# Kernel tuning notes

Measured on AMD Instinct MI355X. Metric: run time of the kernel, lower is better.

Reference implementation:

```python
import jax, jax.numpy as jnp
import numpy as np

B, S, D, O, R, E = 2, 4096, 4096, 4096, 256, 8
SCALE = 2.0

def setup_inputs() -> dict:
    key = jax.random.key(0)
    k_x, k_t, k_w, k_a, k_b = jax.random.split(key, 5)
    x = jax.random.normal(k_x, (B, S, D), dtype=jnp.float32)
    token_type = jax.random.randint(k_t, (S,), 0, E, dtype=jnp.int64)
    # weight_base: [out_features, in_features] as required by F.linear
    weight_base = jax.random.normal(k_w, (O, D), dtype=jnp.float32) * 0.02
    # LoRA stacks: lora_A [E, D, R], lora_B [E, R, O]. (Original inits B to zeros;
    # we use small random values so the LoRA path is numerically non-trivial.)
    lora_A = jax.random.normal(k_a, (E, D, R), dtype=jnp.float32) * 0.02
    lora_B = jax.random.normal(k_b, (E, R, O), dtype=jnp.float32) * 0.02
    return {"x": x, "weight_base": weight_base, "lora_A": lora_A,
            "lora_B": lora_B, "token_type": token_type}

def reference(x, weight_base, lora_A, lora_B, token_type):
    # base GEMM: F.linear(x, W) = x @ W.T  -> [B, S, O]
    base = jnp.einsum('bsd,od->bso', x, weight_base)
    # per-expert low-rank projection: h[e,b,s,:] = x[b,s,:] @ lora_A[e]
    h = jnp.einsum('bsd,edr->ebsr', x, lora_A)              # [E, B, S, R]
    # dispatch: zero out tokens not routed to expert e (token_type partitions S)
    onehot = jax.nn.one_hot(token_type, E, dtype=x.dtype)   # [S, E]
    h = h * onehot.T[:, None, :, None]                      # mask over (e, s)
    # combine: sum over experts of masked h @ lora_B[e]
    lora = jnp.einsum('ebsr,ero->bso', h, lora_B)           # [B, S, O]
    # every token has token_type in [0, E), so scatter covers all positions:
    # result = base + scale * expert_lora everywhere
    return base + SCALE * lora
```

## Files before the change

kernel.cpp:

```cpp
#include <hip/hip_runtime.h>

#define S_TOK 4096
#define D_DIM 4096
#define O_DIM 4096
#define R_DIM 256
#define E_EXP 8
#define NTOK  8192
#define KSPLIT 4

typedef __bf16 bf16x8 __attribute__((ext_vector_type(8)));
typedef float  f32x4  __attribute__((ext_vector_type(4)));

__device__ __forceinline__ unsigned short f2bf(float f) {
  unsigned int u = __float_as_uint(f);
  u += 0x7FFFu + ((u >> 16) & 1u);
  return (unsigned short)(u >> 16);
}
__device__ __forceinline__ float bf2f(unsigned short h) {
  return __uint_as_float(((unsigned int)h) << 16);
}

__device__ __forceinline__ void gload_lds16(const unsigned short* g, unsigned short* l) {
  __builtin_amdgcn_global_load_lds((const __attribute__((address_space(1))) void*)g,
                                   (__attribute__((address_space(3))) void*)l, 16, 0, 0);
}

#define PIPE_FENCE(N)                                                        \
  do {                                                                       \
    asm volatile("s_waitcnt vmcnt(" #N ")\n\ts_barrier" ::: "memory");       \
    __builtin_amdgcn_sched_barrier(0);                                       \
  } while (0)
#define LGKM0                                                                \
  do {                                                                       \
    asm volatile("s_waitcnt lgkmcnt(0)" ::: "memory");                       \
    __builtin_amdgcn_sched_barrier(0);                                       \
  } while (0)
#define SBAR0 __builtin_amdgcn_sched_barrier(0)

__global__ void cast8(const float* __restrict__ in, unsigned short* __restrict__ out) {
  size_t g = (size_t)blockIdx.x * 256 + threadIdx.x;
  const float4* i4 = (const float4*)in;
  float4 a = i4[g * 2], b = i4[g * 2 + 1];
  union { unsigned short h[8]; int4 v; } u;
  u.h[0] = f2bf(a.x); u.h[1] = f2bf(a.y); u.h[2] = f2bf(a.z); u.h[3] = f2bf(a.w);
  u.h[4] = f2bf(b.x); u.h[5] = f2bf(b.y); u.h[6] = f2bf(b.z); u.h[7] = f2bf(b.w);
  ((int4*)out)[g] = u.v;
}

__global__ void transpose_cast(const float* __restrict__ in, unsigned short* __restrict__ out,
                               int P, int Q) {
  __shared__ unsigned short tile[32][33];
  int e = blockIdx.z;
  int pt = blockIdx.x * 32, qt = blockIdx.y * 32;
  const float* ie = in + (size_t)e * P * Q;
  unsigned short* oe = out + (size_t)e * P * Q;
  int tx = threadIdx.x & 31, ty = threadIdx.x >> 5;
  #pragma unroll
  for (int i = 0; i < 32; i += 8) {
    int p = pt + ty + i, q = qt + tx;
    tile[ty + i][tx] = f2bf(ie[(size_t)p * Q + q]);
  }
  __syncthreads();
  #pragma unroll
  for (int i = 0; i < 32; i += 8) {
    int q = qt + ty + i, p = pt + tx;
    oe[(size_t)q * P + p] = tile[tx][ty + i];
  }
}

__global__ void sort_tokens(const int* __restrict__ tt, int* __restrict__ token_perm,
                            int* __restrict__ inv_perm,
                            int* __restrict__ tile_e, int* __restrict__ tile_j0,
                            int* __restrict__ tile_jend, int* __restrict__ ntiles_out) {
  __shared__ int ltt[S_TOK];
  __shared__ int lc[256 * 8];
  __shared__ int basee[8], cnte[8];
  __shared__ int ssl[S_TOK];
  int t = threadIdx.x;
  for (int s = t; s < S_TOK; s += 256) ltt[s] = tt[s];
  __syncthreads();
  int c[8] = {0,0,0,0,0,0,0,0};
  #pragma unroll
  for (int i = 0; i < 16; i++) { int e = ltt[t * 16 + i]; c[e]++; }
  #pragma unroll
  for (int e = 0; e < 8; e++) lc[t * 8 + e] = c[e];
  __syncthreads();
  if (t < 8) {
    int run = 0;
    for (int q = 0; q < 256; q++) { int tmp = lc[q * 8 + t]; lc[q * 8 + t] = run; run += tmp; }
    cnte[t] = run;
  }
  __syncthreads();
  if (t == 0) { int tot = 0; for (int e = 0; e < 8; e++) { basee[e] = tot; tot += cnte[e]; } }
  __syncthreads();
  int off[8];
  #pragma unroll
  for (int e = 0; e < 8; e++) off[e] = basee[e] + lc[t * 8 + e];
  #pragma unroll
  for (int i = 0; i < 16; i++) { int s = t * 16 + i; int e = ltt[s]; ssl[off[e]++] = s; }
  __syncthreads();
  for (int j = t; j < NTOK; j += 256) {
    int row = ((j & 1) << 12) + ssl[j >> 1];
    token_perm[j] = row;
    inv_perm[row] = j;
  }
  if (t == 0) {
    int nt = 0;
    for (int e = 0; e < 8; e++) {
      int js = 2 * basee[e], je = js + 2 * cnte[e];
      for (int j0 = js; j0 < je; j0 += 128) {
        tile_e[nt] = e; tile_j0[nt] = j0;
        tile_jend[nt] = (je < j0 + 128) ? je : (j0 + 128);
        nt++;
      }
    }
    *ntiles_out = nt;
  }
}

template<int FUSED>
__global__ __launch_bounds__(512, 2) void gemm256_dense(
    const unsigned short* __restrict__ A, const unsigned short* __restrict__ B,
    float* __restrict__ C, const unsigned short* __restrict__ lout,
    const int* __restrict__ invp) {
  __shared__ __align__(16) unsigned short ldsA[2][2][8192];
  __shared__ __align__(16) unsigned short ldsB[2][2][8192];
  int b = blockIdx.x;
  int xc = b & 7, q = b >> 3;
  const int bm = (xc >> 1) * 8 + (q >> 3);
  const int bn = (xc & 1) * 8 + (q & 7);
  const int tid = threadIdx.x, l = tid & 63, w = tid >> 6;
  const int wm = w >> 2, wn = w & 3;

  const unsigned short *srcA0, *srcA1, *srcB0, *srcB1;
  {
    int i0 = tid, r0 = i0 >> 2;
    int c0 = ((i0 & 3) * 16) ^ (((r0 >> 1) & 3) << 4);
    srcA0 = A + (size_t)(bm * 256 + r0) * 4096 + (c0 >> 1);
    srcB0 = B + (size_t)(bn * 256 + r0) * 4096 + (c0 >> 1);
    int i1 = 512 + tid, r1 = i1 >> 2;
    int c1 = ((i1 & 3) * 16) ^ (((r1 >> 1) & 3) << 4);
    srcA1 = A + (size_t)(bm * 256 + r1) * 4096 + (c1 >> 1);
    srcB1 = B + (size_t)(bn * 256 + r1) * 4096 + (c1 >> 1);
  }
  const int d0 = tid * 8;

  const int lane15 = l & 15, kb16 = (l >> 4) * 16;
  int offA[8], offB[4];
  #pragma unroll
  for (int m = 0; m < 8; m++) {
    int r = wm * 128 + m * 16 + lane15;
    offA[m] = r * 64 + (kb16 ^ (((r >> 1) & 3) << 4));
  }
  #pragma unroll
  for (int n = 0; n < 4; n++) {
    int r = wn * 64 + n * 16 + lane15;
    offB[n] = r * 64 + (kb16 ^ (((r >> 1) & 3) << 4));
  }

  f32x4 acc[8][4];
  #pragma unroll
  for (int m = 0; m < 8; m++)
    #pragma unroll
    for (int n = 0; n < 4; n++) acc[m][n] = (f32x4){0.f, 0.f, 0.f, 0.f};

  bf16x8 Ab0[4], Ab1[4], Bb0[4], Bb1[4];

#define STAGE_A(tt, kh) do { int _o = (tt) * 64 + (kh) * 32;                  \
    gload_lds16(srcA0 + _o, &ldsA[(tt) & 1][kh][d0]);                         \
    gload_lds16(srcA1 + _o, &ldsA[(tt) & 1][kh][d0 + 4096]); } while (0)
#define STAGE_B(tt, kh) do { int _o = (tt) * 64 + (kh) * 32;                  \
    gload_lds16(srcB0 + _o, &ldsB[(tt) & 1][kh][d0]);                         \
    gload_lds16(srcB1 + _o, &ldsB[(tt) & 1][kh][d0 + 4096]); } while (0)
#define RD_A(RING, QQ, KS, BUF) do {                                          \
    const char* _s = (const char*)&ldsA[RING][KS][0];                         \
    BUF[0] = *(const bf16x8*)(_s + offA[(QQ) * 4 + 0]);                       \
    BUF[1] = *(const bf16x8*)(_s + offA[(QQ) * 4 + 1]);                       \
    BUF[2] = *(const bf16x8*)(_s + offA[(QQ) * 4 + 2]);                       \
    BUF[3] = *(const bf16x8*)(_s + offA[(QQ) * 4 + 3]); } while (0)
#define RD_B(RING, KS, BUF) do {                                              \
    const char* _s = (const char*)&ldsB[RING][KS][0];                         \
    BUF[0] = *(const bf16x8*)(_s + offB[0]);                                  \
    BUF[1] = *(const bf16x8*)(_s + offB[1]);                                  \
    BUF[2] = *(const bf16x8*)(_s + offB[2]);                                  \
    BUF[3] = *(const bf16x8*)(_s + offB[3]); } while (0)
#define PRIO_MFMA(Q, AB, BB) do {                                             \
    __builtin_amdgcn_s_setprio(1);                                            \
    _Pragma("unroll")                                                         \
    for (int mm = 0; mm < 4; mm++)                                            \
      _Pragma("unroll")                                                       \
      for (int nn = 0; nn < 4; nn++)                                          \
        acc[(Q) * 4 + mm][nn] = __builtin_amdgcn_mfma_f32_16x16x32_bf16(      \
            AB[mm], BB[nn], acc[(Q) * 4 + mm][nn], 0, 0, 0);                  \
    __builtin_amdgcn_s_setprio(0); } while (0)

  STAGE_A(0, 0); STAGE_B(0, 0); STAGE_A(0, 1); STAGE_B(0, 1);
  STAGE_A(1, 0); STAGE_B(1, 0);
  PIPE_FENCE(8);
  RD_B(0, 0, Bb0); RD_A(0, 0, 0, Ab0);
  LGKM0;

  #pragma unroll 1
  for (int t = 0; t < 62; ++t) {
    const int r = t & 1, nr = r ^ 1;
    RD_A(r, 1, 0, Ab1); STAGE_A(t + 1, 1); SBAR0;
    PRIO_MFMA(0, Ab0, Bb0);
    LGKM0; PIPE_FENCE(6);
    RD_B(r, 1, Bb1); RD_A(r, 0, 1, Ab0); STAGE_B(t + 1, 1); SBAR0;
    PRIO_MFMA(1, Ab1, Bb0);
    LGKM0; PIPE_FENCE(6);
    RD_A(r, 1, 1, Ab1); STAGE_A(t + 2, 0); SBAR0;
    PRIO_MFMA(0, Ab0, Bb1);
    LGKM0; PIPE_FENCE(6);
    RD_B(nr, 0, Bb0); RD_A(nr, 0, 0, Ab0); STAGE_B(t + 2, 0); SBAR0;
    PRIO_MFMA(1, Ab1, Bb1);
    LGKM0; PIPE_FENCE(6);
  }
  RD_A(0, 1, 0, Ab1); STAGE_A(63, 1); SBAR0; PRIO_MFMA(0, Ab0, Bb0); LGKM0; PIPE_FENCE(6);
  RD_B(0, 1, Bb1); RD_A(0, 0, 1, Ab0); STAGE_B(63, 1); SBAR0; PRIO_MFMA(1, Ab1, Bb0); LGKM0; PIPE_FENCE(6);
  RD_A(0, 1, 1, Ab1); SBAR0; PRIO_MFMA(0, Ab0, Bb1); LGKM0; PIPE_FENCE(4);
  RD_B(1, 0, Bb0); RD_A(1, 0, 0, Ab0); SBAR0; PRIO_MFMA(1, Ab1, Bb1); LGKM0; PIPE_FENCE(4);
  RD_A(1, 1, 0, Ab1); SBAR0; PRIO_MFMA(0, Ab0, Bb0); LGKM0; PIPE_FENCE(0);
  RD_B(1, 1, Bb1); RD_A(1, 0, 1, Ab0); SBAR0; PRIO_MFMA(1, Ab1, Bb0); LGKM0; PIPE_FENCE(0);
  RD_A(1, 1, 1, Ab1); SBAR0; PRIO_MFMA(0, Ab0, Bb1); LGKM0;
  PRIO_MFMA(1, Ab1, Bb1);

#undef STAGE_A
#undef STAGE_B
#undef RD_A
#undef RD_B
#undef PRIO_MFMA

  const int rowbase = bm * 256 + wm * 128;
  const int colbase = bn * 256 + wn * 64;
  #pragma unroll
  for (int m = 0; m < 8; m++)
    #pragma unroll
    for (int v = 0; v < 4; v++) {
      int rrow = rowbase + m * 16 + (l >> 4) * 4 + v;
      float lv0 = 0.f, lv1 = 0.f, lv2 = 0.f, lv3 = 0.f;
      if (FUSED) {
        int jr = invp[rrow];
        const unsigned short* lr = lout + (size_t)jr * O_DIM + colbase + lane15;
        lv0 = bf2f(lr[0]); lv1 = bf2f(lr[16]); lv2 = bf2f(lr[32]); lv3 = bf2f(lr[48]);
      }
      size_t base = (size_t)rrow * O_DIM + colbase + lane15;
      C[base]      = acc[m][0][v] + lv0;
      C[base + 16] = acc[m][1][v] + lv1;
      C[base + 32] = acc[m][2][v] + lv2;
      C[base + 48] = acc[m][3][v] + lv3;
    }
}

template<int MODE>
__global__ __launch_bounds__(256, 2) void gemm_nt(
    const unsigned short* __restrict__ Aop, const unsigned short* __restrict__ Bop,
    float* __restrict__ outF, unsigned short* __restrict__ outU,
    const int* __restrict__ perm, const int* __restrict__ tile_e,
    const int* __restrict__ tile_j0, const int* __restrict__ tile_jend,
    const int* __restrict__ ntiles, int K) {
  int bm = blockIdx.x, bn = blockIdx.y;
  if (bm >= *ntiles) return;
  int e = tile_e[bm], j0 = tile_j0[bm], jend = tile_jend[bm];
  const int kc = (MODE == 1) ? blockIdx.z : 0;
  const int t = threadIdx.x;
  const int l = t & 63, w = t >> 6;
  __shared__ __align__(16) unsigned short lA[128 * 32];
  __shared__ __align__(16) unsigned short lB[128 * 32];

  const unsigned short* srcA[2];
  const unsigned short* srcB[2];
  #pragma unroll
  for (int ck = 0; ck < 2; ck++) {
    int idx = t + ck * 256;
    int lrow = idx >> 2, lk = (idx & 3) * 8;
    int j = j0 + lrow; if (j > jend - 1) j = jend - 1;
    int grow = (MODE == 1) ? perm[j] : j;
    srcA[ck] = Aop + (size_t)grow * K + lk + kc * 1024;
    int bcol = bn * 128 + lrow;
    const unsigned short* bp = Bop;
    if (MODE == 1) bp += (size_t)e * R_DIM * D_DIM;
    else           bp += (size_t)e * O_DIM * R_DIM;
    srcB[ck] = bp + (size_t)bcol * K + lk + kc * 1024;
  }

  f32x4 acc[4][4];
  #pragma unroll
  for (int m = 0; m < 4; m++)
    #pragma unroll
    for (int n = 0; n < 4; n++) acc[m][n] = (f32x4){0.f, 0.f, 0.f, 0.f};

  const int wr = w >> 1, wc = w & 1;
  const int ra = wr * 64 + (l & 15);
  const int rb = wc * 64 + (l & 15);
  const int ko = (l >> 4) * 8;

  const int nk = (MODE == 1) ? (1024 / 32) : (K / 32);
  for (int kt = 0; kt < nk; kt++) {
    __syncthreads();
    #pragma unroll
    for (int ck = 0; ck < 2; ck++) {
      gload_lds16(srcA[ck] + kt * 32, &lA[(w * 64 + ck * 256) * 8]);
      gload_lds16(srcB[ck] + kt * 32, &lB[(w * 64 + ck * 256) * 8]);
    }
    __syncthreads();
    bf16x8 af[4], bfr[4];
    #pragma unroll
    for (int m = 0; m < 4; m++) af[m] = *(const bf16x8*)&lA[(ra + m * 16) * 32 + ko];
    #pragma unroll
    for (int n = 0; n < 4; n++) bfr[n] = *(const bf16x8*)&lB[(rb + n * 16) * 32 + ko];
    #pragma unroll
    for (int m = 0; m < 4; m++)
      #pragma unroll
      for (int n = 0; n < 4; n++)
        acc[m][n] = __builtin_amdgcn_mfma_f32_16x16x32_bf16(af[m], bfr[n], acc[m][n], 0, 0, 0);
  }

  int rowbase = j0 + wr * 64;
  int colbase = bn * 128 + wc * 64;
  #pragma unroll
  for (int m = 0; m < 4; m++) {
    #pragma unroll
    for (int n = 0; n < 4; n++) {
      #pragma unroll
      for (int v = 0; v < 4; v++) {
        int r = rowbase + m * 16 + (l >> 4) * 4 + v;
        int cc = colbase + n * 16 + (l & 15);
        if (r < jend) {
          if (MODE == 1) {
            outU[(size_t)kc * (NTOK * R_DIM) + (size_t)r * R_DIM + cc] = f2bf(acc[m][n][v]);
          } else if (MODE == 2) {
            size_t o = (size_t)perm[r] * O_DIM + cc;
            outF[o] += 2.0f * acc[m][n][v];
          } else {
            outU[(size_t)r * O_DIM + cc] = f2bf(2.0f * acc[m][n][v]);
          }
        }
      }
    }
  }
}

__global__ void reduce_h(const unsigned short* __restrict__ hp, unsigned short* __restrict__ h16) {
  size_t g = (size_t)blockIdx.x * 256 + threadIdx.x;
  float s[8] = {0,0,0,0,0,0,0,0};
  #pragma unroll
  for (int c = 0; c < KSPLIT; c++) {
    int4 v = ((const int4*)hp)[g + (size_t)c * (NTOK * R_DIM / 8)];
    const unsigned short* us = (const unsigned short*)&v;
    #pragma unroll
    for (int i = 0; i < 8; i++) s[i] += bf2f(us[i]);
  }
  union { unsigned short h[8]; int4 v; } u;
  #pragma unroll
  for (int i = 0; i < 8; i++) u.h[i] = f2bf(s[i]);
  ((int4*)h16)[g] = u.v;
}

#define X16_OFF   ((size_t)0)
#define W16_OFF   ((size_t)67108864)
#define A16T_OFF  ((size_t)100663296)
#define B16T_OFF  ((size_t)117440512)
#define H16S_OFF  ((size_t)134217728)
#define PERM_OFF  ((size_t)138412032)
#define INVP_OFF  ((size_t)138444800)
#define TILEE_OFF ((size_t)138477568)
#define TILEJ0_OFF ((size_t)138478080)
#define TILEJE_OFF ((size_t)138478592)
#define NT_OFF    ((size_t)138479104)
#define HP16_OFF  ((size_t)138479616)
#define LOUT_OFF  ((size_t)155256832)
#define WS_FUSED_NEED ((size_t)222365696)

extern "C" void kernel_launch(void* const* d_in, const int* in_sizes, int n_in,
                              void* d_out, int out_size, void* d_ws, size_t ws_size,
                              hipStream_t stream) {
  const float* x  = (const float*)d_in[0];
  const float* wb = (const float*)d_in[1];
  const float* la = (const float*)d_in[2];
  const float* lb = (const float*)d_in[3];
  const int* tok  = (const int*)d_in[4];
  float* out = (float*)d_out;

  char* ws = (char*)d_ws;
  unsigned short* X16  = (unsigned short*)(ws + X16_OFF);
  unsigned short* W16  = (unsigned short*)(ws + W16_OFF);
  unsigned short* A16t = (unsigned short*)(ws + A16T_OFF);
  unsigned short* B16t = (unsigned short*)(ws + B16T_OFF);
  unsigned short* H16s = (unsigned short*)(ws + H16S_OFF);
  int* perm  = (int*)(ws + PERM_OFF);
  int* invp  = (int*)(ws + INVP_OFF);
  int* tl_e  = (int*)(ws + TILEE_OFF);
  int* tl_j0 = (int*)(ws + TILEJ0_OFF);
  int* tl_je = (int*)(ws + TILEJE_OFF);
  int* nt    = (int*)(ws + NT_OFF);

  const bool fused = ws_size >= WS_FUSED_NEED;

  cast8<<<16384, 256, 0, stream>>>(x, X16);
  cast8<<<8192, 256, 0, stream>>>(wb, W16);
  transpose_cast<<<dim3(128, 8, 8), 256, 0, stream>>>(la, A16t, D_DIM, R_DIM);
  transpose_cast<<<dim3(8, 128, 8), 256, 0, stream>>>(lb, B16t, R_DIM, O_DIM);
  sort_tokens<<<1, 256, 0, stream>>>(tok, perm, invp, tl_e, tl_j0, tl_je, nt);

  if (fused) {
    unsigned short* HP16 = (unsigned short*)(ws + HP16_OFF);
    unsigned short* LOUT = (unsigned short*)(ws + LOUT_OFF);
    gemm_nt<1><<<dim3(71, 2, KSPLIT), 256, 0, stream>>>(X16, A16t, nullptr, HP16,
                                                        perm, tl_e, tl_j0, tl_je, nt, D_DIM);
    reduce_h<<<1024, 256, 0, stream>>>(HP16, H16s);
    gemm_nt<3><<<dim3(71, 32), 256, 0, stream>>>(H16s, B16t, nullptr, LOUT,
                                                 perm, tl_e, tl_j0, tl_je, nt, R_DIM);
    gemm256_dense<1><<<512, 512, 0, stream>>>(X16, W16, out, LOUT, invp);
  } else {
    unsigned short* HP16 = (unsigned short*)(ws + W16_OFF);
    gemm256_dense<0><<<512, 512, 0, stream>>>(X16, W16, out, nullptr, nullptr);
    gemm_nt<1><<<dim3(71, 2, KSPLIT), 256, 0, stream>>>(X16, A16t, nullptr, HP16,
                                                        perm, tl_e, tl_j0, tl_je, nt, D_DIM);
    reduce_h<<<1024, 256, 0, stream>>>(HP16, H16s);
    gemm_nt<2><<<dim3(71, 32), 256, 0, stream>>>(H16s, B16t, out, nullptr,
                                                 perm, tl_e, tl_j0, tl_je, nt, R_DIM);
  }
}
```

Measured before the change: 460.0 us.

## Use partial lgkmcnt waits and halve global-load barriers in GEMM main loop

The main loop no longer waits for all LDS reads (lgkmcnt(0)) before each MFMA block. It uses partial lgkmcnt waits so that only the fragments the next MFMA needs must have arrived, letting later LDS reads overlap with compute. The vmcnt+s_barrier fence now runs twice per iteration instead of four times, with adjusted counts, which cuts workgroup barrier stalls. The trade-off is a more fragile ordering of LDS ring-buffer reads and writes, where a wrong count could cause data races.

```diff
diff --git a/kernel.cpp b/kernel.cpp
--- a/kernel.cpp
+++ b/kernel.cpp
@@ -30,9 +30,9 @@
     asm volatile("s_waitcnt vmcnt(" #N ")\n\ts_barrier" ::: "memory");       \
     __builtin_amdgcn_sched_barrier(0);                                       \
   } while (0)
-#define LGKM0                                                                \
+#define LGKMC(N)                                                             \
   do {                                                                       \
-    asm volatile("s_waitcnt lgkmcnt(0)" ::: "memory");                       \
+    asm volatile("s_waitcnt lgkmcnt(" #N ")" ::: "memory");                  \
     __builtin_amdgcn_sched_barrier(0);                                       \
   } while (0)
 #define SBAR0 __builtin_amdgcn_sched_barrier(0)
@@ -196,34 +196,34 @@
 
   STAGE_A(0, 0); STAGE_B(0, 0); STAGE_A(0, 1); STAGE_B(0, 1);
   STAGE_A(1, 0); STAGE_B(1, 0);
-  PIPE_FENCE(8);
+  PIPE_FENCE(4);
   RD_B(0, 0, Bb0); RD_A(0, 0, 0, Ab0);
-  LGKM0;
+  SBAR0;
 
   #pragma unroll 1
   for (int t = 0; t < 62; ++t) {
     const int r = t & 1, nr = r ^ 1;
-    RD_A(r, 1, 0, Ab1); STAGE_A(t + 1, 1); SBAR0;
+    RD_A(r, 1, 0, Ab1); SBAR0; STAGE_A(t + 1, 1); SBAR0; LGKMC(4);
     PRIO_MFMA(0, Ab0, Bb0);
-    LGKM0; PIPE_FENCE(6);
-    RD_B(r, 1, Bb1); RD_A(r, 0, 1, Ab0); STAGE_B(t + 1, 1); SBAR0;
+    RD_B(r, 1, Bb1); RD_A(r, 0, 1, Ab0); SBAR0; STAGE_B(t + 1, 1); SBAR0; LGKMC(8);
     PRIO_MFMA(1, Ab1, Bb0);
-    LGKM0; PIPE_FENCE(6);
-    RD_A(r, 1, 1, Ab1); STAGE_A(t + 2, 0); SBAR0;
+    PIPE_FENCE(4);
+    RD_A(r, 1, 1, Ab1); SBAR0; STAGE_A(t + 2, 0); SBAR0; LGKMC(4);
     PRIO_MFMA(0, Ab0, Bb1);
-    LGKM0; PIPE_FENCE(6);
-    RD_B(nr, 0, Bb0); RD_A(nr, 0, 0, Ab0); STAGE_B(t + 2, 0); SBAR0;
+    RD_B(nr, 0, Bb0); RD_A(nr, 0, 0, Ab0); SBAR0; STAGE_B(t + 2, 0); SBAR0; LGKMC(8);
     PRIO_MFMA(1, Ab1, Bb1);
-    LGKM0; PIPE_FENCE(6);
-  }
-  RD_A(0, 1, 0, Ab1); STAGE_A(63, 1); SBAR0; PRIO_MFMA(0, Ab0, Bb0); LGKM0; PIPE_FENCE(6);
-  RD_B(0, 1, Bb1); RD_A(0, 0, 1, Ab0); STAGE_B(63, 1); SBAR0; PRIO_MFMA(1, Ab1, Bb0); LGKM0; PIPE_FENCE(6);
-  RD_A(0, 1, 1, Ab1); SBAR0; PRIO_MFMA(0, Ab0, Bb1); LGKM0; PIPE_FENCE(4);
-  RD_B(1, 0, Bb0); RD_A(1, 0, 0, Ab0); SBAR0; PRIO_MFMA(1, Ab1, Bb1); LGKM0; PIPE_FENCE(4);
-  RD_A(1, 1, 0, Ab1); SBAR0; PRIO_MFMA(0, Ab0, Bb0); LGKM0; PIPE_FENCE(0);
-  RD_B(1, 1, Bb1); RD_A(1, 0, 1, Ab0); SBAR0; PRIO_MFMA(1, Ab1, Bb0); LGKM0; PIPE_FENCE(0);
-  RD_A(1, 1, 1, Ab1); SBAR0; PRIO_MFMA(0, Ab0, Bb1); LGKM0;
-  PRIO_MFMA(1, Ab1, Bb1);
+    PIPE_FENCE(4);
+  }
+  RD_A(0, 1, 0, Ab1); SBAR0; STAGE_A(63, 1); SBAR0; LGKMC(4); PRIO_MFMA(0, Ab0, Bb0);
+  RD_B(0, 1, Bb1); RD_A(0, 0, 1, Ab0); SBAR0; STAGE_B(63, 1); SBAR0; LGKMC(8);
+  PRIO_MFMA(1, Ab1, Bb0); PIPE_FENCE(4);
+  RD_A(0, 1, 1, Ab1); SBAR0; LGKMC(4); PRIO_MFMA(0, Ab0, Bb1);
+  RD_B(1, 0, Bb0); RD_A(1, 0, 0, Ab0); SBAR0; LGKMC(8); PRIO_MFMA(1, Ab1, Bb1);
+  PIPE_FENCE(0);
+  RD_A(1, 1, 0, Ab1); SBAR0; LGKMC(4); PRIO_MFMA(0, Ab0, Bb0);
+  RD_B(1, 1, Bb1); RD_A(1, 0, 1, Ab0); SBAR0; LGKMC(8); PRIO_MFMA(1, Ab1, Bb0);
+  RD_A(1, 1, 1, Ab1); SBAR0; LGKMC(4); PRIO_MFMA(0, Ab0, Bb1);
+  LGKMC(0); PRIO_MFMA(1, Ab1, Bb1);
 
 #undef STAGE_A
 #undef STAGE_B
```

Result: no change. 456.9 us (-0.7%).
